# Kernel tuning notes

Hardware: AMD Instinct MI355X
Metric: run time of the kernel (lower is better)

The kernel has to match this reference:

```python
import jax, jax.numpy as jnp
import numpy as np

B, OBS, DH, N, DK, DV, TASKS, OUT = 4096, 512, 1024, 8, 256, 1024, 10, 128
LOG_SIG_MIN, LOG_SIG_MAX = -20.0, 2.0


def _lin(k, fan_in, shape):
    return jax.random.normal(k, shape, jnp.float32) / np.sqrt(fan_in)


def setup_inputs() -> dict:
    ks = jax.random.split(jax.random.key(0), 18)
    return {
        "x": jax.random.normal(ks[0], (B, OBS), jnp.float32),
        "task_id": 3,
        # base MLP (2 layers)
        "Wb1": _lin(ks[1], OBS, (OBS, DH)), "bb1": jnp.zeros((DH,), jnp.float32),
        "Wb2": _lin(ks[2], DH, (DH, DH)), "bb2": jnp.zeros((DH,), jnp.float32),
        # per-expert MLPs (stacked over expert dim n)
        "We1": _lin(ks[3], DH, (N, DH, DH)), "be1": jnp.zeros((N, DH), jnp.float32),
        "We2": _lin(ks[4], DH, (N, DH, DH)), "be2": jnp.zeros((N, DH), jnp.float32),
        # per-expert attention v / k heads
        "Wv": _lin(ks[5], DH, (N, DH, DV)), "bv": jnp.zeros((N, DV), jnp.float32),
        "Wk": _lin(ks[6], DH, (N, DH, DK)), "bk": jnp.zeros((N, DK), jnp.float32),
        # per-task q networks (input = one-hot task vector of size TASKS)
        "Wq": _lin(ks[7], TASKS, (TASKS, TASKS, DK)), "bq": jnp.zeros((TASKS, DK), jnp.float32),
        # tower + last
        "Wt1": _lin(ks[8], DV, (DV, DH)), "bt1": jnp.zeros((DH,), jnp.float32),
        "Wl": _lin(ks[9], DH, (DH, OUT)) * 0.003, "bl": jnp.zeros((OUT,), jnp.float32),
    }


def reference(x, task_id, Wb1, bb1, Wb2, bb2, We1, be1, We2, be2,
              Wv, bv, Wk, bk, Wq, bq, Wt1, bt1, Wl, bl):
    act = jax.nn.relu
    # base: [B, DH]
    h = act(act(x @ Wb1 + bb1) @ Wb2 + bb2)
    # all experts at once: e [N, B, DH]
    e = act(jnp.einsum('bd,ndh->nbh', h, We1) + be1[:, None, :])
    e = act(jnp.einsum('nbd,ndh->nbh', e, We2) + be2[:, None, :])
    # attention values / keys per expert
    v = jnp.einsum('nbd,ndv->nbv', e, Wv) + bv[:, None, :]   # [N, B, DV]
    k = jnp.einsum('nbd,ndk->nbk', e, Wk) + bk[:, None, :]   # [N, B, DK]
    # q from one-hot task index through task-specific q net
    task_idx = jax.nn.one_hot(task_id, TASKS, dtype=x.dtype)  # [TASKS]
    q = task_idx @ Wq[task_id] + bq[task_id]                  # [DK]
    # raw (unnormalized) weights, as in the original (alphas are computed but unused)
    expkq = jnp.einsum('nbk,k->nb', k, q)                     # [N, B]
    res = jnp.einsum('nbv,nb->bv', v, expkq)                  # [B, DV]
    t = act(res @ Wt1 + bt1)
    out = t @ Wl + bl                                          # [B, OUT]
    mean, log_std = jnp.split(out, 2, axis=-1)
    log_std = jnp.clip(log_std, LOG_SIG_MIN, LOG_SIG_MAX)
    std = jnp.exp(log_std)
    return mean, std, log_std
```

## Files before the change

kernel.cpp:

```cpp
#include <hip/hip_runtime.h>
#include <hip/hip_bf16.h>

typedef unsigned short u16;
typedef unsigned int   u32;
typedef __attribute__((ext_vector_type(4))) float  f32x4;
typedef __attribute__((ext_vector_type(8))) __bf16 bf16x8;

#define B_    4096
#define OBS_  512
#define DH_   1024
#define NEXP_ 8
#define DK_   256
#define DV_   1024

__device__ __forceinline__ float b2f(u32 lo16) {
  return __builtin_bit_cast(float, lo16 << 16);
}
__device__ __forceinline__ u16 f2b(float f) {
  u32 u = __builtin_bit_cast(u32, f);
  return (u16)((u + 0x7fffu + ((u >> 16) & 1u)) >> 16);
}
__device__ __forceinline__ void gl_lds16(const u16* g, u16* l) {
  __builtin_amdgcn_global_load_lds(
      (__attribute__((address_space(1))) void*)(void*)g,
      (__attribute__((address_space(3))) void*)(void*)l,
      16, 0, 0);
}

__device__ __forceinline__ void tconv_body(const float* __restrict__ in,
                                           u16* __restrict__ outp,
                                           int R, int C, int rem, int tid) {
  __shared__ float tile[32][33];
  int gxs = (C == 128) ? 2 : 5;
  int c0 = (rem & ((1 << gxs) - 1)) * 32;
  int r0 = (rem >> gxs) * 32;
  int tx = tid & 31, ty = tid >> 5;
#pragma unroll
  for (int i = 0; i < 4; ++i)
    tile[ty + i * 8][tx] = in[(long)(r0 + ty + i * 8) * C + c0 + tx];
  __syncthreads();
#pragma unroll
  for (int i = 0; i < 4; ++i)
    outp[(long)(c0 + ty + i * 8) * R + r0 + tx] = f2b(tile[tx][ty + i * 8]);
}

__global__ __launch_bounds__(256)
void prep(const float* __restrict__ x,  u16* __restrict__ xb,
          const float* __restrict__ Wb1, u16* __restrict__ Wb1T,
          const float* __restrict__ Wb2, u16* __restrict__ Wb2T,
          const float* __restrict__ We1, u16* __restrict__ We1T,
          const float* __restrict__ We2, u16* __restrict__ We2T,
          const float* __restrict__ Wv,  u16* __restrict__ WvT,
          const float* __restrict__ Wt1, u16* __restrict__ Wt1T,
          const float* __restrict__ Wl,  u16* __restrict__ WlT,
          const float* __restrict__ Wq,  const float* __restrict__ bq,
          const float* __restrict__ bk,  const int* __restrict__ task,
          const float* __restrict__ Wk,  float* __restrict__ wnq,
          float* __restrict__ cn) {
  int tid = threadIdx.x;
  int bid = blockIdx.x;
  if (bid < 2048) {
    long i = ((long)bid * 256 + tid) * 4;
    float4 v = *(const float4*)(x + i);
    u16 o[4] = { f2b(v.x), f2b(v.y), f2b(v.z), f2b(v.w) };
    *(uint2*)(xb + i) = *(const uint2*)o;
    return;
  }
  bid -= 2048;
  if (bid < 512)  { tconv_body(Wb1, Wb1T, 512, 1024, bid, tid); return; }
  bid -= 512;
  if (bid < 1024) { tconv_body(Wb2, Wb2T, 1024, 1024, bid, tid); return; }
  bid -= 1024;
  if (bid < 8192) {
    int z = bid >> 10, rem = bid & 1023;
    tconv_body(We1 + (long)z * DH_ * DH_, We1T + (long)z * DH_ * DH_, 1024, 1024, rem, tid);
    return;
  }
  bid -= 8192;
  if (bid < 8192) {
    int z = bid >> 10, rem = bid & 1023;
    tconv_body(We2 + (long)z * DH_ * DH_, We2T + (long)z * DH_ * DH_, 1024, 1024, rem, tid);
    return;
  }
  bid -= 8192;
  if (bid < 8192) { tconv_body(Wv, WvT, 8192, 1024, bid, tid); return; }
  bid -= 8192;
  if (bid < 1024) { tconv_body(Wt1, Wt1T, 1024, 1024, bid, tid); return; }
  bid -= 1024;
  if (bid < 128)  { tconv_body(Wl, WlT, 1024, 128, bid, tid); return; }
  bid -= 128;
  int t = *task;
  const float* qrow = Wq + (long)(t * 10 + t) * DK_;
  const float* brow = bq + (long)t * DK_;
  int lane = tid & 63;
  if (bid < 2048) {
    int row = bid * 4 + (tid >> 6);
    const float* wr = Wk + (long)row * DK_;
    float s = 0.f;
#pragma unroll
    for (int i = 0; i < 4; ++i) {
      int j = lane + i * 64;
      s += wr[j] * (qrow[j] + brow[j]);
    }
    for (int off = 32; off; off >>= 1) s += __shfl_xor(s, off);
    if (lane == 0) wnq[row] = s;
  } else {
    int w = tid >> 6;
    for (int n = w; n < NEXP_; n += 4) {
      float s = 0.f;
#pragma unroll
      for (int i = 0; i < 4; ++i) {
        int j = lane + i * 64;
        s += bk[n * DK_ + j] * (qrow[j] + brow[j]);
      }
      for (int off = 32; off; off >>= 1) s += __shfl_xor(s, off);
      if (lane == 0) cn[n] = s;
    }
  }
}

template<int RELU, int OUT, int EKQ, int LDA, int LDB>
__global__ __launch_bounds__(256, 4)
void gemm_bt(const u16* __restrict__ A, const u16* __restrict__ Bt,
             const float* __restrict__ bias, void* __restrict__ Cv,
             int M, int N, int kper, int ksplit,
             long aB, long bB, long biasB, long cB,
             const float* __restrict__ wnq, float* __restrict__ ekqPart) {
  const int zz = blockIdx.z;
  const int split = zz % ksplit;
  const int batch = zz / ksplit;
  A  += (long)batch * aB + (long)split * kper;
  Bt += (long)batch * bB + (long)split * kper;

  int m_idx = blockIdx.y, n_idx = blockIdx.x;
  if (gridDim.x == 8) {
    int f = blockIdx.x + (blockIdx.y << 3);
    int xcd = f & 7, j = f >> 3;
    n_idx = j & 7;
    m_idx = (xcd << 2) | (j >> 3);
  }
  const int m0 = m_idx * 128, n0 = n_idx * 128;

  __shared__ u16 As[128 * 64];
  __shared__ u16 Bs[128 * 64];
  const int tid  = threadIdx.x;
  const int lane = tid & 63, wid = tid >> 6;
  const int wm = (wid >> 1) * 64, wn = (wid & 1) * 64;
  const int lr = lane & 15, quad = lane >> 4;
  const int srow = lane >> 3;
  const int scol = ((lane & 7) ^ srow) * 8;

  const u16* ap0 = A  + (long)(m0 + wid * 32 +  0 + srow) * LDA + scol;
  const u16* ap1 = A  + (long)(m0 + wid * 32 +  8 + srow) * LDA + scol;
  const u16* ap2 = A  + (long)(m0 + wid * 32 + 16 + srow) * LDA + scol;
  const u16* ap3 = A  + (long)(m0 + wid * 32 + 24 + srow) * LDA + scol;
  const u16* bp0 = Bt + (long)(n0 + wid * 32 +  0 + srow) * LDB + scol;
  const u16* bp1 = Bt + (long)(n0 + wid * 32 +  8 + srow) * LDB + scol;
  const u16* bp2 = Bt + (long)(n0 + wid * 32 + 16 + srow) * LDB + scol;
  const u16* bp3 = Bt + (long)(n0 + wid * 32 + 24 + srow) * LDB + scol;
  u16* la = &As[wid * 2048];
  u16* lb = &Bs[wid * 2048];

  const int rsw = lr & 7;
  const int aB0 = (wm + lr) * 64 + ((quad    ) ^ rsw) * 8;
  const int aB1 = (wm + lr) * 64 + ((quad + 4) ^ rsw) * 8;
  const int bB0 = (wn + lr) * 64 + ((quad    ) ^ rsw) * 8;
  const int bB1 = (wn + lr) * 64 + ((quad + 4) ^ rsw) * 8;

  f32x4 acc[4][4] = {};

  for (int k0 = 0; k0 < kper; k0 += 64) {
    __syncthreads();
    gl_lds16(ap0 + k0, la);        gl_lds16(ap1 + k0, la + 512);
    gl_lds16(ap2 + k0, la + 1024); gl_lds16(ap3 + k0, la + 1536);
    gl_lds16(bp0 + k0, lb);        gl_lds16(bp1 + k0, lb + 512);
    gl_lds16(bp2 + k0, lb + 1024); gl_lds16(bp3 + k0, lb + 1536);
    __syncthreads();
#pragma unroll
    for (int h = 0; h < 2; ++h) {
      const int ab = h ? aB1 : aB0, bb = h ? bB1 : bB0;
      bf16x8 af[4], bfr[4];
#pragma unroll
      for (int i = 0; i < 4; ++i) af[i]  = *(const bf16x8*)(&As[ab + i * 1024]);
#pragma unroll
      for (int i = 0; i < 4; ++i) bfr[i] = *(const bf16x8*)(&Bs[bb + i * 1024]);
#pragma unroll
      for (int mi = 0; mi < 4; ++mi)
#pragma unroll
        for (int ni = 0; ni < 4; ++ni)
          acc[mi][ni] = __builtin_amdgcn_mfma_f32_16x16x32_bf16(af[mi], bfr[ni], acc[mi][ni], 0, 0, 0);
    }
  }

  if (OUT == 1) {
    float* C = (float*)Cv + (long)split * ((long)M * N);
#pragma unroll
    for (int mi = 0; mi < 4; ++mi)
#pragma unroll
      for (int ni = 0; ni < 4; ++ni) {
        int col = n0 + wn + ni * 16 + lr;
#pragma unroll
        for (int r = 0; r < 4; ++r) {
          int row = m0 + wm + mi * 16 + quad * 4 + r;
          C[(long)row * N + col] = acc[mi][ni][r];
        }
      }
  } else {
    u16* C = (u16*)Cv + (long)batch * cB;
    const float* bptr = bias ? bias + (long)batch * biasB : nullptr;
    float* eLds = (float*)As;
    if (EKQ) __syncthreads();
#pragma unroll
    for (int mi = 0; mi < 4; ++mi) {
      float psum[4] = {0.f, 0.f, 0.f, 0.f};
#pragma unroll
      for (int ni = 0; ni < 4; ++ni) {
        int col = n0 + wn + ni * 16 + lr;
        float bcol = bptr ? bptr[col] : 0.f;
        float wq = EKQ ? wnq[(long)batch * N + col] : 0.f;
#pragma unroll
        for (int r = 0; r < 4; ++r) {
          int row = m0 + wm + mi * 16 + quad * 4 + r;
          float v = acc[mi][ni][r] + bcol;
          if (RELU) v = fmaxf(v, 0.f);
          C[(long)row * N + col] = f2b(v);
          if (EKQ) psum[r] += v * wq;
        }
      }
      if (EKQ) {
#pragma unroll
        for (int r = 0; r < 4; ++r) {
          float s = psum[r];
          s += __shfl_xor(s, 1); s += __shfl_xor(s, 2);
          s += __shfl_xor(s, 4); s += __shfl_xor(s, 8);
          if (lr == 0) eLds[wid * 64 + mi * 16 + quad * 4 + r] = s;
        }
      }
    }
    if (EKQ) {
      __syncthreads();
      if (tid < 128) {
        int half = tid >> 6, loc = tid & 63;
        float v = eLds[half * 128 + loc] + eLds[half * 128 + 64 + loc];
        ekqPart[((long)batch * 8 + n_idx) * M + m0 + tid] = v;
      }
    }
  }
}

template<int LDA, int LDB>
__global__ __launch_bounds__(256, 4)
void gemm_sm(const u16* __restrict__ A, const u16* __restrict__ Bt,
             const float* __restrict__ bias, u16* __restrict__ C,
             int N, int kper) {
  int f = blockIdx.x + (blockIdx.y << 3);
  int xcd = f & 7;
  const int n_idx = (f >> 3) & 7;
  const int m_idx = (xcd << 3) | (f >> 6);
  const int m0 = m_idx * 64, n0 = n_idx * 128;

  __shared__ u16 As[64 * 64];
  __shared__ u16 Bs[128 * 64];
  const int tid  = threadIdx.x;
  const int lane = tid & 63, wid = tid >> 6;
  const int wn = wid * 32;
  const int lr = lane & 15, quad = lane >> 4;
  const int srow = lane >> 3;
  const int scol = ((lane & 7) ^ srow) * 8;

  const u16* ap0 = A  + (long)(m0 + wid * 16 + 0 + srow) * LDA + scol;
  const u16* ap1 = A  + (long)(m0 + wid * 16 + 8 + srow) * LDA + scol;
  const u16* bp0 = Bt + (long)(n0 + wid * 32 +  0 + srow) * LDB + scol;
  const u16* bp1 = Bt + (long)(n0 + wid * 32 +  8 + srow) * LDB + scol;
  const u16* bp2 = Bt + (long)(n0 + wid * 32 + 16 + srow) * LDB + scol;
  const u16* bp3 = Bt + (long)(n0 + wid * 32 + 24 + srow) * LDB + scol;
  u16* la = &As[wid * 1024];
  u16* lb = &Bs[wid * 2048];

  const int rsw = lr & 7;
  const int aB0 = lr * 64 + ((quad    ) ^ rsw) * 8;
  const int aB1 = lr * 64 + ((quad + 4) ^ rsw) * 8;
  const int bB0 = (wn + lr) * 64 + ((quad    ) ^ rsw) * 8;
  const int bB1 = (wn + lr) * 64 + ((quad + 4) ^ rsw) * 8;

  f32x4 acc[4][2] = {};

  for (int k0 = 0; k0 < kper; k0 += 64) {
    __syncthreads();
    gl_lds16(ap0 + k0, la);        gl_lds16(ap1 + k0, la + 512);
    gl_lds16(bp0 + k0, lb);        gl_lds16(bp1 + k0, lb + 512);
    gl_lds16(bp2 + k0, lb + 1024); gl_lds16(bp3 + k0, lb + 1536);
    __syncthreads();
#pragma unroll
    for (int h = 0; h < 2; ++h) {
      const int ab = h ? aB1 : aB0, bb = h ? bB1 : bB0;
      bf16x8 af[4], bfr[2];
#pragma unroll
      for (int i = 0; i < 4; ++i) af[i]  = *(const bf16x8*)(&As[ab + i * 1024]);
#pragma unroll
      for (int i = 0; i < 2; ++i) bfr[i] = *(const bf16x8*)(&Bs[bb + i * 1024]);
#pragma unroll
      for (int mi = 0; mi < 4; ++mi)
#pragma unroll
        for (int ni = 0; ni < 2; ++ni)
          acc[mi][ni] = __builtin_amdgcn_mfma_f32_16x16x32_bf16(af[mi], bfr[ni], acc[mi][ni], 0, 0, 0);
    }
  }

#pragma unroll
  for (int mi = 0; mi < 4; ++mi)
#pragma unroll
    for (int ni = 0; ni < 2; ++ni) {
      int col = n0 + wn + ni * 16 + lr;
      float bcol = bias[col];
#pragma unroll
      for (int r = 0; r < 4; ++r) {
        int row = m0 + mi * 16 + quad * 4 + r;
        C[(long)row * N + col] = f2b(fmaxf(acc[mi][ni][r] + bcol, 0.f));
      }
    }
}

__global__ __launch_bounds__(256)
void reduce_res(const u16* __restrict__ y, const float* __restrict__ ekqPart,
                const float* __restrict__ cn, const float* __restrict__ bvp,
                u16* __restrict__ res) {
  long f8 = ((long)blockIdx.x * 256 + threadIdx.x) * 8;
  int b = (int)(f8 >> 10);
  int v = (int)(f8 & (DV_ - 1));
  float s[NEXP_];
#pragma unroll
  for (int n = 0; n < NEXP_; ++n) {
    float t = cn[n];
#pragma unroll
    for (int nt = 0; nt < 8; ++nt) t += ekqPart[((long)n * 8 + nt) * B_ + b];
    s[n] = t;
  }
  float acc[8] = {};
#pragma unroll
  for (int n = 0; n < NEXP_; ++n) {
    float sn = s[n];
    uint4 p = *(const uint4*)(y + ((long)(n * B_ + b) * DV_) + v);
    const u32* pi = (const u32*)&p;
    float4 b0 = *(const float4*)(bvp + n * DV_ + v);
    float4 b1 = *(const float4*)(bvp + n * DV_ + v + 4);
    acc[0] += sn * (b2f(pi[0] & 0xffffu) + b0.x);
    acc[1] += sn * (b2f(pi[0] >> 16)     + b0.y);
    acc[2] += sn * (b2f(pi[1] & 0xffffu) + b0.z);
    acc[3] += sn * (b2f(pi[1] >> 16)     + b0.w);
    acc[4] += sn * (b2f(pi[2] & 0xffffu) + b1.x);
    acc[5] += sn * (b2f(pi[2] >> 16)     + b1.y);
    acc[6] += sn * (b2f(pi[3] & 0xffffu) + b1.z);
    acc[7] += sn * (b2f(pi[3] >> 16)     + b1.w);
  }
  u16 o[8];
#pragma unroll
  for (int i = 0; i < 8; ++i) o[i] = f2b(acc[i]);
  *(uint4*)(res + f8) = *(const uint4*)o;
}

__global__ __launch_bounds__(256)
void reduce_final(const float* __restrict__ part, const float* __restrict__ bl,
                  float* __restrict__ outp) {
  int flat = blockIdx.x * 256 + threadIdx.x;
  int c = flat & 127, b = flat >> 7;
  float v = bl[c];
  const long S = (long)B_ * 128;
#pragma unroll
  for (int s = 0; s < 8; ++s) v += part[s * S + flat];
  if (c < 64) {
    outp[b * 64 + c] = v;
  } else {
    int i = b * 64 + (c - 64);
    float ls = fminf(fmaxf(v, -20.f), 2.f);
    outp[262144 + i] = expf(ls);
    outp[524288 + i] = ls;
  }
}

extern "C" void kernel_launch(void* const* d_in, const int* in_sizes, int n_in,
                              void* d_out, int out_size, void* d_ws, size_t ws_size,
                              hipStream_t stream) {
  const float* x   = (const float*)d_in[0];
  const int*   task= (const int*)  d_in[1];
  const float* Wb1 = (const float*)d_in[2];
  const float* bb1 = (const float*)d_in[3];
  const float* Wb2 = (const float*)d_in[4];
  const float* bb2 = (const float*)d_in[5];
  const float* We1 = (const float*)d_in[6];
  const float* be1 = (const float*)d_in[7];
  const float* We2 = (const float*)d_in[8];
  const float* be2 = (const float*)d_in[9];
  const float* Wv  = (const float*)d_in[10];
  const float* bv  = (const float*)d_in[11];
  const float* Wk  = (const float*)d_in[12];
  const float* bk  = (const float*)d_in[13];
  const float* Wq  = (const float*)d_in[14];
  const float* bq  = (const float*)d_in[15];
  const float* Wt1 = (const float*)d_in[16];
  const float* bt1 = (const float*)d_in[17];
  const float* Wl  = (const float*)d_in[18];
  const float* bl  = (const float*)d_in[19];
  float* outp = (float*)d_out;

  char* ws = (char*)d_ws;
  size_t off = 0;
  auto alloc = [&](size_t bytes) -> char* {
    char* p = ws + off;
    off += (bytes + 255) & ~(size_t)255;
    return p;
  };

  u16* xb    = (u16*)alloc((size_t)B_ * OBS_ * 2);
  u16* Wb1T  = (u16*)alloc((size_t)DH_ * OBS_ * 2);
  u16* Wb2T  = (u16*)alloc((size_t)DH_ * DH_ * 2);
  u16* We1T  = (u16*)alloc((size_t)NEXP_ * DH_ * DH_ * 2);
  u16* We2T  = (u16*)alloc((size_t)NEXP_ * DH_ * DH_ * 2);
  u16* WvT   = (u16*)alloc((size_t)DV_ * NEXP_ * DH_ * 2);
  u16* Wt1T  = (u16*)alloc((size_t)DH_ * DV_ * 2);
  u16* WlT   = (u16*)alloc((size_t)128 * DH_ * 2);
  u16* h1    = (u16*)alloc((size_t)B_ * DH_ * 2);
  u16* h     = (u16*)alloc((size_t)B_ * DH_ * 2);
  u16* e1    = (u16*)alloc((size_t)NEXP_ * B_ * DH_ * 2);
  u16* e2    = (u16*)alloc((size_t)NEXP_ * B_ * DH_ * 2);
  float* cn  = (float*)alloc(NEXP_ * 4);
  float* wnq = (float*)alloc((size_t)NEXP_ * DH_ * 4);
  float* ekqPart = (float*)alloc((size_t)NEXP_ * 8 * B_ * 4);
  u16*   y     = e1;
  u16*   res   = h1;
  u16*   tt    = h;
  float* partB = (float*)e2;

  prep<<<31361, 256, 0, stream>>>(x, xb, Wb1, Wb1T, Wb2, Wb2T, We1, We1T,
                                  We2, We2T, Wv, WvT, Wt1, Wt1T, Wl, WlT,
                                  Wq, bq, bk, task, Wk, wnq, cn);

  gemm_sm<OBS_, OBS_><<<dim3(8, 64), 256, 0, stream>>>(xb, Wb1T, bb1, h1, DH_, OBS_);
  gemm_sm<DH_, DH_><<<dim3(8, 64), 256, 0, stream>>>(h1, Wb2T, bb2, h, DH_, DH_);
  gemm_bt<1, 0, 0, DH_, DH_><<<dim3(8, 32, 8), 256, 0, stream>>>(h, We1T, be1, e1,
      B_, DH_, DH_, 1, 0, (long)DH_ * DH_, DH_, (long)B_ * DH_, nullptr, nullptr);
  gemm_bt<1, 0, 1, DH_, DH_><<<dim3(8, 32, 8), 256, 0, stream>>>(e1, We2T, be2, e2,
      B_, DH_, DH_, 1, (long)B_ * DH_, (long)DH_ * DH_, DH_, (long)B_ * DH_, wnq, ekqPart);
  gemm_bt<0, 0, 0, DH_, NEXP_ * DH_><<<dim3(8, 32, 8), 256, 0, stream>>>(e2, WvT, nullptr, y,
      B_, DV_, DH_, 1, (long)B_ * DH_, DH_, 0, (long)B_ * DV_, nullptr, nullptr);
  reduce_res<<<2048, 256, 0, stream>>>(y, ekqPart, cn, bv, res);
  gemm_sm<DV_, DV_><<<dim3(8, 64), 256, 0, stream>>>(res, Wt1T, bt1, tt, DH_, DV_);
  gemm_bt<0, 1, 0, DH_, DH_><<<dim3(1, 32, 8), 256, 0, stream>>>(tt, WlT, nullptr, partB,
      B_, 128, 128, 8, 0, 0, 0, 0, nullptr, nullptr);
  reduce_final<<<(B_ * 128) / 256, 256, 0, stream>>>(partB, bl, outp);
}
```

Measured before the change: 458.0 us.

## Stagger K-loop start per block and fuse last GEMM with output epilogue

Measured after the change: 496.5 us. 1.08x slower.

```diff
diff --git a/kernel.cpp b/kernel.cpp
--- a/kernel.cpp
+++ b/kernel.cpp
@@ -119,26 +119,21 @@
   }
 }
 
-template<int RELU, int OUT, int EKQ, int LDA, int LDB>
+template<int RELU, int EKQ, int LDA, int LDB>
 __global__ __launch_bounds__(256, 4)
 void gemm_bt(const u16* __restrict__ A, const u16* __restrict__ Bt,
-             const float* __restrict__ bias, void* __restrict__ Cv,
-             int M, int N, int kper, int ksplit,
+             const float* __restrict__ bias, u16* __restrict__ C,
+             int M, int N, int kper,
              long aB, long bB, long biasB, long cB,
              const float* __restrict__ wnq, float* __restrict__ ekqPart) {
-  const int zz = blockIdx.z;
-  const int split = zz % ksplit;
-  const int batch = zz / ksplit;
-  A  += (long)batch * aB + (long)split * kper;
-  Bt += (long)batch * bB + (long)split * kper;
-
-  int m_idx = blockIdx.y, n_idx = blockIdx.x;
-  if (gridDim.x == 8) {
-    int f = blockIdx.x + (blockIdx.y << 3);
-    int xcd = f & 7, j = f >> 3;
-    n_idx = j & 7;
-    m_idx = (xcd << 2) | (j >> 3);
-  }
+  const int batch = blockIdx.z;
+  A  += (long)batch * aB;
+  Bt += (long)batch * bB;
+
+  int f = blockIdx.x + (blockIdx.y << 3);
+  int xcd = f & 7, j = f >> 3;
+  const int n_idx = j & 7;
+  const int m_idx = (xcd << 2) | (j >> 3);
   const int m0 = m_idx * 128, n0 = n_idx * 128;
 
   __shared__ u16 As[128 * 64];
@@ -169,7 +164,11 @@
 
   f32x4 acc[4][4] = {};
 
-  for (int k0 = 0; k0 < kper; k0 += 64) {
+  const int kmask  = kper - 1;
+  const int kstart = ((j + batch * 5) * 64) & kmask;
+
+  for (int i = 0; i < kper; i += 64) {
+    const int k0 = (kstart + i) & kmask;
     __syncthreads();
     gl_lds16(ap0 + k0, la);        gl_lds16(ap1 + k0, la + 512);
     gl_lds16(ap2 + k0, la + 1024); gl_lds16(ap3 + k0, la + 1536);
@@ -181,9 +180,9 @@
       const int ab = h ? aB1 : aB0, bb = h ? bB1 : bB0;
       bf16x8 af[4], bfr[4];
 #pragma unroll
-      for (int i = 0; i < 4; ++i) af[i]  = *(const bf16x8*)(&As[ab + i * 1024]);
-#pragma unroll
-      for (int i = 0; i < 4; ++i) bfr[i] = *(const bf16x8*)(&Bs[bb + i * 1024]);
+      for (int i2 = 0; i2 < 4; ++i2) af[i2]  = *(const bf16x8*)(&As[ab + i2 * 1024]);
+#pragma unroll
+      for (int i2 = 0; i2 < 4; ++i2) bfr[i2] = *(const bf16x8*)(&Bs[bb + i2 * 1024]);
 #pragma unroll
       for (int mi = 0; mi < 4; ++mi)
 #pragma unroll
@@ -192,58 +191,43 @@
     }
   }
 
-  if (OUT == 1) {
-    float* C = (float*)Cv + (long)split * ((long)M * N);
-#pragma unroll
-    for (int mi = 0; mi < 4; ++mi)
-#pragma unroll
-      for (int ni = 0; ni < 4; ++ni) {
-        int col = n0 + wn + ni * 16 + lr;
-#pragma unroll
-        for (int r = 0; r < 4; ++r) {
-          int row = m0 + wm + mi * 16 + quad * 4 + r;
-          C[(long)row * N + col] = acc[mi][ni][r];
-        }
+  u16* Cb = C + (long)batch * cB;
+  const float* bptr = bias ? bias + (long)batch * biasB : nullptr;
+  float* eLds = (float*)As;
+  if (EKQ) __syncthreads();
+#pragma unroll
+  for (int mi = 0; mi < 4; ++mi) {
+    float psum[4] = {0.f, 0.f, 0.f, 0.f};
+#pragma unroll
+    for (int ni = 0; ni < 4; ++ni) {
+      int col = n0 + wn + ni * 16 + lr;
+      float bcol = bptr ? bptr[col] : 0.f;
+      float wq = EKQ ? wnq[(long)batch * N + col] : 0.f;
+#pragma unroll
+      for (int r = 0; r < 4; ++r) {
+        int row = m0 + wm + mi * 16 + quad * 4 + r;
+        float v = acc[mi][ni][r] + bcol;
+        if (RELU) v = fmaxf(v, 0.f);
+        Cb[(long)row * N + col] = f2b(v);
+        if (EKQ) psum[r] += v * wq;
       }
-  } else {
-    u16* C = (u16*)Cv + (long)batch * cB;
-    const float* bptr = bias ? bias + (long)batch * biasB : nullptr;
-    float* eLds = (float*)As;
-    if (EKQ) __syncthreads();
-#pragma unroll
-    for (int mi = 0; mi < 4; ++mi) {
-      float psum[4] = {0.f, 0.f, 0.f, 0.f};
-#pragma unroll
-      for (int ni = 0; ni < 4; ++ni) {
-        int col = n0 + wn + ni * 16 + lr;
-        float bcol = bptr ? bptr[col] : 0.f;
-        float wq = EKQ ? wnq[(long)batch * N + col] : 0.f;
-#pragma unroll
-        for (int r = 0; r < 4; ++r) {
-          int row = m0 + wm + mi * 16 + quad * 4 + r;
-          float v = acc[mi][ni][r] + bcol;
-          if (RELU) v = fmaxf(v, 0.f);
-          C[(long)row * N + col] = f2b(v);
-          if (EKQ) psum[r] += v * wq;
-        }
+    }
+    if (EKQ) {
+#pragma unroll
+      for (int r = 0; r < 4; ++r) {
+        float s = psum[r];
+        s += __shfl_xor(s, 1); s += __shfl_xor(s, 2);
+        s += __shfl_xor(s, 4); s += __shfl_xor(s, 8);
+        if (lr == 0) eLds[wid * 64 + mi * 16 + quad * 4 + r] = s;
       }
-      if (EKQ) {
-#pragma unroll
-        for (int r = 0; r < 4; ++r) {
-          float s = psum[r];
-          s += __shfl_xor(s, 1); s += __shfl_xor(s, 2);
-          s += __shfl_xor(s, 4); s += __shfl_xor(s, 8);
-          if (lr == 0) eLds[wid * 64 + mi * 16 + quad * 4 + r] = s;
-        }
-      }
-    }
-    if (EKQ) {
-      __syncthreads();
-      if (tid < 128) {
-        int half = tid >> 6, loc = tid & 63;
-        float v = eLds[half * 128 + loc] + eLds[half * 128 + 64 + loc];
-        ekqPart[((long)batch * 8 + n_idx) * M + m0 + tid] = v;
-      }
+    }
+  }
+  if (EKQ) {
+    __syncthreads();
+    if (tid < 128) {
+      int half = tid >> 6, loc = tid & 63;
+      float v = eLds[half * 128 + loc] + eLds[half * 128 + 64 + loc];
+      ekqPart[((long)batch * 8 + n_idx) * M + m0 + tid] = v;
     }
   }
 }
@@ -285,7 +269,11 @@
 
   f32x4 acc[4][2] = {};
 
-  for (int k0 = 0; k0 < kper; k0 += 64) {
+  const int kmask  = kper - 1;
+  const int kstart = (f * 64) & kmask;
+
+  for (int i = 0; i < kper; i += 64) {
+    const int k0 = (kstart + i) & kmask;
     __syncthreads();
     gl_lds16(ap0 + k0, la);        gl_lds16(ap1 + k0, la + 512);
     gl_lds16(bp0 + k0, lb);        gl_lds16(bp1 + k0, lb + 512);
@@ -296,9 +284,9 @@
       const int ab = h ? aB1 : aB0, bb = h ? bB1 : bB0;
       bf16x8 af[4], bfr[2];
 #pragma unroll
-      for (int i = 0; i < 4; ++i) af[i]  = *(const bf16x8*)(&As[ab + i * 1024]);
-#pragma unroll
-      for (int i = 0; i < 2; ++i) bfr[i] = *(const bf16x8*)(&Bs[bb + i * 1024]);
+      for (int i2 = 0; i2 < 4; ++i2) af[i2]  = *(const bf16x8*)(&As[ab + i2 * 1024]);
+#pragma unroll
+      for (int i2 = 0; i2 < 2; ++i2) bfr[i2] = *(const bf16x8*)(&Bs[bb + i2 * 1024]);
 #pragma unroll
       for (int mi = 0; mi < 4; ++mi)
 #pragma unroll
@@ -317,6 +305,84 @@
       for (int r = 0; r < 4; ++r) {
         int row = m0 + mi * 16 + quad * 4 + r;
         C[(long)row * N + col] = f2b(fmaxf(acc[mi][ni][r] + bcol, 0.f));
+      }
+    }
+}
+
+__global__ __launch_bounds__(256, 4)
+void gemm_last(const u16* __restrict__ A, const u16* __restrict__ Bt,
+               const float* __restrict__ bl, float* __restrict__ outp,
+               int kper) {
+  const int m0 = blockIdx.x * 32;
+  __shared__ u16 As[32 * 64];
+  __shared__ u16 Bs[128 * 64];
+  const int tid  = threadIdx.x;
+  const int lane = tid & 63, wid = tid >> 6;
+  const int wn = wid * 32;
+  const int lr = lane & 15, quad = lane >> 4;
+  const int srow = lane >> 3;
+  const int scol = ((lane & 7) ^ srow) * 8;
+
+  const u16* ap0 = A  + (long)(m0 + wid * 8 + srow) * DH_ + scol;
+  const u16* bp0 = Bt + (long)(wid * 32 +  0 + srow) * DH_ + scol;
+  const u16* bp1 = Bt + (long)(wid * 32 +  8 + srow) * DH_ + scol;
+  const u16* bp2 = Bt + (long)(wid * 32 + 16 + srow) * DH_ + scol;
+  const u16* bp3 = Bt + (long)(wid * 32 + 24 + srow) * DH_ + scol;
+  u16* la = &As[wid * 512];
+  u16* lb = &Bs[wid * 2048];
+
+  const int rsw = lr & 7;
+  const int aB0 = lr * 64 + ((quad    ) ^ rsw) * 8;
+  const int aB1 = lr * 64 + ((quad + 4) ^ rsw) * 8;
+  const int bB0 = (wn + lr) * 64 + ((quad    ) ^ rsw) * 8;
+  const int bB1 = (wn + lr) * 64 + ((quad + 4) ^ rsw) * 8;
+
+  f32x4 acc[2][2] = {};
+
+  const int kmask  = kper - 1;
+  const int kstart = (blockIdx.x * 64) & kmask;
+
+  for (int i = 0; i < kper; i += 64) {
+    const int k0 = (kstart + i) & kmask;
+    __syncthreads();
+    gl_lds16(ap0 + k0, la);
+    gl_lds16(bp0 + k0, lb);        gl_lds16(bp1 + k0, lb + 512);
+    gl_lds16(bp2 + k0, lb + 1024); gl_lds16(bp3 + k0, lb + 1536);
+    __syncthreads();
+#pragma unroll
+    for (int h = 0; h < 2; ++h) {
+      const int ab = h ? aB1 : aB0, bb = h ? bB1 : bB0;
+      bf16x8 af[2], bfr[2];
+#pragma unroll
+      for (int i2 = 0; i2 < 2; ++i2) af[i2]  = *(const bf16x8*)(&As[ab + i2 * 1024]);
+#pragma unroll
+      for (int i2 = 0; i2 < 2; ++i2) bfr[i2] = *(const bf16x8*)(&Bs[bb + i2 * 1024]);
+#pragma unroll
+      for (int mi = 0; mi < 2; ++mi)
+#pragma unroll
+        for (int ni = 0; ni < 2; ++ni)
+          acc[mi][ni] = __builtin_amdgcn_mfma_f32_16x16x32_bf16(af[mi], bfr[ni], acc[mi][ni], 0, 0, 0);
+    }
+  }
+
+#pragma unroll
+  for (int mi = 0; mi < 2; ++mi)
+#pragma unroll
+    for (int ni = 0; ni < 2; ++ni) {
+      int col = wn + ni * 16 + lr;
+      float bcol = bl[col];
+#pragma unroll
+      for (int r = 0; r < 4; ++r) {
+        int row = m0 + mi * 16 + quad * 4 + r;
+        float v = acc[mi][ni][r] + bcol;
+        if (col < 64) {
+          outp[(long)row * 64 + col] = v;
+        } else {
+          float ls = fminf(fmaxf(v, -20.f), 2.f);
+          long idx = (long)row * 64 + (col - 64);
+          outp[262144 + idx] = expf(ls);
+          outp[524288 + idx] = ls;
+        }
       }
     }
 }
@@ -357,25 +423,6 @@
 #pragma unroll
   for (int i = 0; i < 8; ++i) o[i] = f2b(acc[i]);
   *(uint4*)(res + f8) = *(const uint4*)o;
-}
-
-__global__ __launch_bounds__(256)
-void reduce_final(const float* __restrict__ part, const float* __restrict__ bl,
-                  float* __restrict__ outp) {
-  int flat = blockIdx.x * 256 + threadIdx.x;
-  int c = flat & 127, b = flat >> 7;
-  float v = bl[c];
-  const long S = (long)B_ * 128;
-#pragma unroll
-  for (int s = 0; s < 8; ++s) v += part[s * S + flat];
-  if (c < 64) {
-    outp[b * 64 + c] = v;
-  } else {
-    int i = b * 64 + (c - 64);
-    float ls = fminf(fmaxf(v, -20.f), 2.f);
-    outp[262144 + i] = expf(ls);
-    outp[524288 + i] = ls;
-  }
 }
 
 extern "C" void kernel_launch(void* const* d_in, const int* in_sizes, int n_in,
@@ -429,7 +476,6 @@
   u16*   y     = e1;
   u16*   res   = h1;
   u16*   tt    = h;
-  float* partB = (float*)e2;
 
   prep<<<31361, 256, 0, stream>>>(x, xb, Wb1, Wb1T, Wb2, Wb2T, We1, We1T,
                                   We2, We2T, Wv, WvT, Wt1, Wt1T, Wl, WlT,
@@ -437,15 +483,13 @@
 
   gemm_sm<OBS_, OBS_><<<dim3(8, 64), 256, 0, stream>>>(xb, Wb1T, bb1, h1, DH_, OBS_);
   gemm_sm<DH_, DH_><<<dim3(8, 64), 256, 0, stream>>>(h1, Wb2T, bb2, h, DH_, DH_);
-  gemm_bt<1, 0, 0, DH_, DH_><<<dim3(8, 32, 8), 256, 0, stream>>>(h, We1T, be1, e1,
-      B_, DH_, DH_, 1, 0, (long)DH_ * DH_, DH_, (long)B_ * DH_, nullptr, nullptr);
-  gemm_bt<1, 0, 1, DH_, DH_><<<dim3(8, 32, 8), 256, 0, stream>>>(e1, We2T, be2, e2,
-      B_, DH_, DH_, 1, (long)B_ * DH_, (long)DH_ * DH_, DH_, (long)B_ * DH_, wnq, ekqPart);
-  gemm_bt<0, 0, 0, DH_, NEXP_ * DH_><<<dim3(8, 32, 8), 256, 0, stream>>>(e2, WvT, nullptr, y,
-      B_, DV_, DH_, 1, (long)B_ * DH_, DH_, 0, (long)B_ * DV_, nullptr, nullptr);
+  gemm_bt<1, 0, DH_, DH_><<<dim3(8, 32, 8), 256, 0, stream>>>(h, We1T, be1, e1,
+      B_, DH_, DH_, 0, (long)DH_ * DH_, DH_, (long)B_ * DH_, nullptr, nullptr);
+  gemm_bt<1, 1, DH_, DH_><<<dim3(8, 32, 8), 256, 0, stream>>>(e1, We2T, be2, e2,
+      B_, DH_, DH_, (long)B_ * DH_, (long)DH_ * DH_, DH_, (long)B_ * DH_, wnq, ekqPart);
+  gemm_bt<0, 0, DH_, NEXP_ * DH_><<<dim3(8, 32, 8), 256, 0, stream>>>(e2, WvT, nullptr, y,
+      B_, DV_, DH_, (long)B_ * DH_, DH_, 0, (long)B_ * DV_, nullptr, nullptr);
   reduce_res<<<2048, 256, 0, stream>>>(y, ekqPart, cn, bv, res);
   gemm_sm<DV_, DV_><<<dim3(8, 64), 256, 0, stream>>>(res, Wt1T, bt1, tt, DH_, DV_);
-  gemm_bt<0, 1, 0, DH_, DH_><<<dim3(1, 32, 8), 256, 0, stream>>>(tt, WlT, nullptr, partB,
-      B_, 128, 128, 8, 0, 0, 0, 0, nullptr, nullptr);
-  reduce_final<<<(B_ * 128) / 256, 256, 0, stream>>>(partB, bl, outp);
-}
+  gemm_last<<<128, 256, 0, stream>>>(tt, WlT, bl, outp, DH_);
+}
```
